# Optimization experiments

Measured on AMD Instinct MI355X. Metric: run time of the kernel, lower is better.

## Reference

```python
import jax, jax.numpy as jnp
import numpy as np

# Conv2d_mvm config (matches init_kwargs): the bit-sliced crossbar MVM is a
# fixed-point emulation of an exact stride-1 conv2d with padding=1, no bias.
C_IN, C_OUT, K, H, W, PAD = 16, 16, 3, 1024, 1024, 1


def setup_inputs() -> dict:
    key = jax.random.key(0)
    kx, kw = jax.random.split(key)
    x = jax.random.normal(kx, (1, C_IN, H, W), dtype=jnp.float32)
    # kaiming_uniform-style init for the conv weight
    fan_in = C_IN * K * K
    bound = 1.0 / np.sqrt(fan_in)
    weight = jax.random.uniform(kw, (C_OUT, C_IN, K, K), dtype=jnp.float32,
                                minval=-bound, maxval=bound)
    return {"x": x, "weight": weight}


def reference(x, weight):
    # Ideal math of the bit-sliced crossbar MVM: per output pixel, the
    # flattened (C_in*K*K) receptive field dotted with each flattened filter.
    out = jax.lax.conv_general_dilated(
        x, weight,
        window_strides=(1, 1),
        padding=((PAD, PAD), (PAD, PAD)),
        dimension_numbers=("NCHW", "OIHW", "NCHW"),
    )
    # Original forward returns (C_out, H_out, W_out) with batch=1 assumed.
    return out[0]
```

## Files before the change

### kernel.cpp

```cpp
#include <hip/hip_runtime.h>


#define H 1024
#define W 1024
#define HW (H * W)
#define TW 128
#define TH 4
#define LROWS 6
#define NQ 34
#define NJOBS (LROWS * NQ)
#define LCOLS 130
#define LPITCH (LCOLS * 32)
#define LDS_BYTES (LROWS * LPITCH)

typedef __bf16 bf16x8 __attribute__((ext_vector_type(8)));
typedef float f32x4 __attribute__((ext_vector_type(4)));
typedef unsigned short ushort8 __attribute__((ext_vector_type(8)));
typedef unsigned int uint4v __attribute__((ext_vector_type(4)));

__device__ __host__ inline unsigned short f2bf(float f) {
  unsigned u = __builtin_bit_cast(unsigned, f);
  return (unsigned short)((u + 0x7fffu + ((u >> 16) & 1u)) >> 16);
}

__global__ __launch_bounds__(256) void conv_prep(const float* __restrict__ w,
                                                 unsigned short* __restrict__ wA) {
  int i = blockIdx.x * 256 + threadIdx.x;
  if (i >= 5 * 64 * 8) return;
  int j = i & 7;
  int l = (i >> 3) & 63;
  int p = i >> 9;
  int k = (l >> 4) * 8 + j;
  int t = 2 * p + (k >> 4);
  int ci = k & 15;
  int co = l & 15;
  float v = (t <= 8) ? w[co * 144 + ci * 9 + t] : 0.f;
  wA[i] = f2bf(v);
}

__device__ __forceinline__ void stage_job(int j, const float* __restrict__ x,
                                          int colbase, int rowbase, char* lds) {
  const int ly  = j / NQ;
  const int qx  = j - ly * NQ;
  const int gy  = rowbase - 1 + ly;
  const float rowm = ((unsigned)gy < (unsigned)H) ? 1.f : 0.f;
  const int gyc  = gy < 0 ? 0 : (gy > H - 1 ? H - 1 : gy);
  const int gx0  = colbase - 4 + 4 * qx;
  const int gx0c = gx0 < 0 ? 0 : (gx0 > W - 4 ? W - 4 : gx0);
  const unsigned voff = (unsigned)((gyc * W + gx0c) * 4);

  f32x4 L[16];
  asm volatile(
      "global_load_dwordx4 %0, %8, %9\n\t"
      "global_load_dwordx4 %1, %8, %10\n\t"
      "global_load_dwordx4 %2, %8, %11\n\t"
      "global_load_dwordx4 %3, %8, %12\n\t"
      "global_load_dwordx4 %4, %8, %13\n\t"
      "global_load_dwordx4 %5, %8, %14\n\t"
      "global_load_dwordx4 %6, %8, %15\n\t"
      "global_load_dwordx4 %7, %8, %16\n\t"
      : "=&v"(L[0]), "=&v"(L[1]), "=&v"(L[2]), "=&v"(L[3]),
        "=&v"(L[4]), "=&v"(L[5]), "=&v"(L[6]), "=&v"(L[7])
      : "v"(voff), "s"(x), "s"(x + HW), "s"(x + 2 * HW), "s"(x + 3 * HW),
        "s"(x + 4 * HW), "s"(x + 5 * HW), "s"(x + 6 * HW), "s"(x + 7 * HW));
  asm volatile(
      "global_load_dwordx4 %0, %8, %9\n\t"
      "global_load_dwordx4 %1, %8, %10\n\t"
      "global_load_dwordx4 %2, %8, %11\n\t"
      "global_load_dwordx4 %3, %8, %12\n\t"
      "global_load_dwordx4 %4, %8, %13\n\t"
      "global_load_dwordx4 %5, %8, %14\n\t"
      "global_load_dwordx4 %6, %8, %15\n\t"
      "global_load_dwordx4 %7, %8, %16\n\t"
      : "=&v"(L[8]), "=&v"(L[9]), "=&v"(L[10]), "=&v"(L[11]),
        "=&v"(L[12]), "=&v"(L[13]), "=&v"(L[14]), "=&v"(L[15])
      : "v"(voff), "s"(x + 8 * HW), "s"(x + 9 * HW), "s"(x + 10 * HW),
        "s"(x + 11 * HW), "s"(x + 12 * HW), "s"(x + 13 * HW),
        "s"(x + 14 * HW), "s"(x + 15 * HW));

  asm volatile("s_waitcnt vmcnt(0)" ::: "memory");
  __builtin_amdgcn_sched_barrier(0);

#pragma unroll
  for (int i = 0; i < 4; ++i) {
    const int gx = gx0 + i;
    const int lx = gx - (colbase - 1);
    if ((unsigned)lx < (unsigned)LCOLS) {
      const float fm = rowm * (((unsigned)gx < (unsigned)W) ? 1.f : 0.f);
      const int lb = (ly * LPITCH + lx * 32) ^ (((lx >> 2) & 3) << 4);
#pragma unroll
      for (int h = 0; h < 2; ++h) {
        uint4v d;
#pragma unroll
        for (int p = 0; p < 4; ++p) {
          const unsigned lo = f2bf(L[h * 8 + 2 * p][i] * fm);
          const unsigned hi = f2bf(L[h * 8 + 2 * p + 1][i] * fm);
          d[p] = lo | (hi << 16);
        }
        *(uint4v*)(lds + (lb ^ (h << 4))) = d;
      }
    }
  }
}

__global__ __launch_bounds__(256, 6) void conv_mfma(
    const float* __restrict__ x, const unsigned short* __restrict__ wA,
    float* __restrict__ out) {
  __shared__ __align__(16) char lds[LDS_BYTES];

  const int tid  = threadIdx.x;
  const int lane = tid & 63;
  const int wave = tid >> 6;
  const int m = lane & 15;
  const int q = lane >> 4;
  const int colbase = blockIdx.x * TW;
  const int rowbase = blockIdx.y * TH;

  if (tid < NJOBS) stage_job(tid, x, colbase, rowbase, lds);

  ushort8 wU[5];
#pragma unroll
  for (int p = 0; p < 5; ++p)
    wU[p] = *(const ushort8*)&wA[(p * 64 + lane) * 8];

  int baseaddr[5];
#pragma unroll
  for (int p = 0; p < 5; ++p) {
    int t = 2 * p + (q >> 1);
    int ky = 0, kx = 0;
    if (t <= 8) { ky = t / 3; kx = t - ky * 3; }
    int col = m + kx;
    int b = ky * LPITCH + col * 32 + (q & 1) * 16;
    b ^= ((col >> 2) & 3) << 4;
    baseaddr[p] = b + wave * LPITCH;
  }

  __syncthreads();

#pragma unroll
  for (int g = 0; g < 8; ++g) {
    f32x4 acc = {0.f, 0.f, 0.f, 0.f};
#pragma unroll
    for (int p = 0; p < 5; ++p) {
      ushort8 bU = *(const ushort8*)(lds + (baseaddr[p] + g * 512));
      acc = __builtin_amdgcn_mfma_f32_16x16x32_bf16(
          __builtin_bit_cast(bf16x8, bU),
          __builtin_bit_cast(bf16x8, wU[p]),
          acc, 0, 0, 0);
    }
    const int y  = rowbase + wave;
    const int x0 = colbase + g * 16 + q * 4;
    *(f32x4*)(out + m * HW + y * W + x0) = acc;
  }
}

extern "C" void kernel_launch(void* const* d_in, const int* in_sizes, int n_in,
                              void* d_out, int out_size, void* d_ws, size_t ws_size,
                              hipStream_t stream) {
  const float* x = (const float*)d_in[0];
  const float* w = (const float*)d_in[1];
  float* out = (float*)d_out;
  unsigned short* wA = (unsigned short*)d_ws;

  conv_prep<<<10, 256, 0, stream>>>(w, wA);

  dim3 grid(W / TW, H / TH);
  conv_mfma<<<grid, 256, 0, stream>>>(x, wA, out);
}
```

Measured before the change: 37.29 us.

## Process two row tiles per block and prefetch the second tile during compute

Each block now handles two vertically adjacent 4-row tiles, so the grid is halved. The global loads for the second tile are issued before the first tile's MFMA compute, which hides their latency behind that compute. Weight loads become inline-asm global loads, and explicit waitcnt and s_barrier calls control the LDS reuse between the two tiles. Launch bounds drop from 6 to 4 waves per SIMD, and the partial vmcnt wait assumes the vector-memory counter completes in order while the output stores are still outstanding.

```diff
diff --git a/kernel.cpp b/kernel.cpp
--- a/kernel.cpp
+++ b/kernel.cpp
@@ -6,6 +6,7 @@
 #define HW (H * W)
 #define TW 128
 #define TH 4
+#define NT 2
 #define LROWS 6
 #define NQ 34
 #define NJOBS (LROWS * NQ)
@@ -38,18 +39,9 @@
   wA[i] = f2bf(v);
 }
 
-__device__ __forceinline__ void stage_job(int j, const float* __restrict__ x,
-                                          int colbase, int rowbase, char* lds) {
-  const int ly  = j / NQ;
-  const int qx  = j - ly * NQ;
-  const int gy  = rowbase - 1 + ly;
-  const float rowm = ((unsigned)gy < (unsigned)H) ? 1.f : 0.f;
-  const int gyc  = gy < 0 ? 0 : (gy > H - 1 ? H - 1 : gy);
-  const int gx0  = colbase - 4 + 4 * qx;
-  const int gx0c = gx0 < 0 ? 0 : (gx0 > W - 4 ? W - 4 : gx0);
-  const unsigned voff = (unsigned)((gyc * W + gx0c) * 4);
-
-  f32x4 L[16];
+__device__ __forceinline__ void issue16(f32x4 (&L)[16],
+                                        const float* __restrict__ x,
+                                        unsigned voff) {
   asm volatile(
       "global_load_dwordx4 %0, %8, %9\n\t"
       "global_load_dwordx4 %1, %8, %10\n\t"
@@ -62,7 +54,8 @@
       : "=&v"(L[0]), "=&v"(L[1]), "=&v"(L[2]), "=&v"(L[3]),
         "=&v"(L[4]), "=&v"(L[5]), "=&v"(L[6]), "=&v"(L[7])
       : "v"(voff), "s"(x), "s"(x + HW), "s"(x + 2 * HW), "s"(x + 3 * HW),
-        "s"(x + 4 * HW), "s"(x + 5 * HW), "s"(x + 6 * HW), "s"(x + 7 * HW));
+        "s"(x + 4 * HW), "s"(x + 5 * HW), "s"(x + 6 * HW), "s"(x + 7 * HW)
+      : "memory");
   asm volatile(
       "global_load_dwordx4 %0, %8, %9\n\t"
       "global_load_dwordx4 %1, %8, %10\n\t"
@@ -76,11 +69,12 @@
         "=&v"(L[12]), "=&v"(L[13]), "=&v"(L[14]), "=&v"(L[15])
       : "v"(voff), "s"(x + 8 * HW), "s"(x + 9 * HW), "s"(x + 10 * HW),
         "s"(x + 11 * HW), "s"(x + 12 * HW), "s"(x + 13 * HW),
-        "s"(x + 14 * HW), "s"(x + 15 * HW));
-
-  asm volatile("s_waitcnt vmcnt(0)" ::: "memory");
-  __builtin_amdgcn_sched_barrier(0);
-
+        "s"(x + 14 * HW), "s"(x + 15 * HW)
+      : "memory");
+}
+
+__device__ __forceinline__ void pack16(const f32x4 (&L)[16], float rowm, int ly,
+                                       int gx0, int colbase, char* lds) {
 #pragma unroll
   for (int i = 0; i < 4; ++i) {
     const int gx = gx0 + i;
@@ -103,7 +97,7 @@
   }
 }
 
-__global__ __launch_bounds__(256, 6) void conv_mfma(
+__global__ __launch_bounds__(256, 4) void conv_mfma(
     const float* __restrict__ x, const unsigned short* __restrict__ wA,
     float* __restrict__ out) {
   __shared__ __align__(16) char lds[LDS_BYTES];
@@ -113,15 +107,43 @@
   const int wave = tid >> 6;
   const int m = lane & 15;
   const int q = lane >> 4;
-  const int colbase = blockIdx.x * TW;
-  const int rowbase = blockIdx.y * TH;
-
-  if (tid < NJOBS) stage_job(tid, x, colbase, rowbase, lds);
+  const int colbase  = blockIdx.x * TW;
+  const int rowbase0 = blockIdx.y * (TH * NT);
+
+  const bool st = tid < NJOBS;
+  int ly = 0, gx0 = 0, gx0c = 0;
+  if (st) {
+    ly = tid / NQ;
+    const int qx = tid - ly * NQ;
+    gx0  = colbase - 4 + 4 * qx;
+    gx0c = gx0 < 0 ? 0 : (gx0 > W - 4 ? W - 4 : gx0);
+  }
+  auto tile_off = [&](int rowbase, float& rm) -> unsigned {
+    const int gy = rowbase - 1 + ly;
+    rm = ((unsigned)gy < (unsigned)H) ? 1.f : 0.f;
+    const int gyc = gy < 0 ? 0 : (gy > H - 1 ? H - 1 : gy);
+    return (unsigned)((gyc * W + gx0c) * 4);
+  };
+
+  f32x4 L[16];
+  float rowm;
+  const unsigned voff0 = tile_off(rowbase0, rowm);
+  if (st) issue16(L, x, voff0);
 
   ushort8 wU[5];
-#pragma unroll
-  for (int p = 0; p < 5; ++p)
-    wU[p] = *(const ushort8*)&wA[(p * 64 + lane) * 8];
+  {
+    const unsigned wvoff = (unsigned)(lane * 16);
+    asm volatile(
+        "global_load_dwordx4 %0, %5, %6\n\t"
+        "global_load_dwordx4 %1, %5, %7\n\t"
+        "global_load_dwordx4 %2, %5, %8\n\t"
+        "global_load_dwordx4 %3, %5, %9\n\t"
+        "global_load_dwordx4 %4, %5, %10\n\t"
+        : "=&v"(wU[0]), "=&v"(wU[1]), "=&v"(wU[2]), "=&v"(wU[3]), "=&v"(wU[4])
+        : "v"(wvoff), "s"(wA), "s"(wA + 512), "s"(wA + 1024), "s"(wA + 1536),
+          "s"(wA + 2048)
+        : "memory");
+  }
 
   int baseaddr[5];
 #pragma unroll
@@ -135,23 +157,42 @@
     baseaddr[p] = b + wave * LPITCH;
   }
 
-  __syncthreads();
-
-#pragma unroll
-  for (int g = 0; g < 8; ++g) {
-    f32x4 acc = {0.f, 0.f, 0.f, 0.f};
-#pragma unroll
-    for (int p = 0; p < 5; ++p) {
-      ushort8 bU = *(const ushort8*)(lds + (baseaddr[p] + g * 512));
-      acc = __builtin_amdgcn_mfma_f32_16x16x32_bf16(
-          __builtin_bit_cast(bf16x8, bU),
-          __builtin_bit_cast(bf16x8, wU[p]),
-          acc, 0, 0, 0);
-    }
-    const int y  = rowbase + wave;
-    const int x0 = colbase + g * 16 + q * 4;
-    *(f32x4*)(out + m * HW + y * W + x0) = acc;
-  }
+  asm volatile("s_waitcnt vmcnt(0)" ::: "memory");
+  __builtin_amdgcn_sched_barrier(0);
+  if (st) pack16(L, rowm, ly, gx0, colbase, lds);
+  asm volatile("s_waitcnt lgkmcnt(0)" ::: "memory");
+  asm volatile("s_barrier" ::: "memory");
+
+#define COMPUTE(RB)                                                         \
+  {                                                                         \
+    const int y = (RB) + wave;                                              \
+    float* const orow = out + m * HW + y * W + colbase + q * 4;             \
+    _Pragma("unroll") for (int g = 0; g < 8; ++g) {                         \
+      f32x4 acc = {0.f, 0.f, 0.f, 0.f};                                     \
+      _Pragma("unroll") for (int p = 0; p < 5; ++p) {                       \
+        const ushort8 bU =                                                  \
+            *(const ushort8*)(lds + (baseaddr[p] + g * 512));               \
+        acc = __builtin_amdgcn_mfma_f32_16x16x32_bf16(                      \
+            __builtin_bit_cast(bf16x8, bU),                \
+            __builtin_bit_cast(bf16x8, wU[p]),             \
+            acc, 0, 0, 0);                                                  \
+      }                                                                     \
+      *(f32x4*)(orow + g * 16) = acc;                                       \
+    }                                                                       \
+  }
+
+  const unsigned voff1 = tile_off(rowbase0 + TH, rowm);
+  if (st) issue16(L, x, voff1);
+  COMPUTE(rowbase0);
+  asm volatile("s_barrier" ::: "memory");
+  asm volatile("s_waitcnt vmcnt(8)" ::: "memory");
+  __builtin_amdgcn_sched_barrier(0);
+  if (st) pack16(L, rowm, ly, gx0, colbase, lds);
+  asm volatile("s_waitcnt lgkmcnt(0)" ::: "memory");
+  asm volatile("s_barrier" ::: "memory");
+  COMPUTE(rowbase0 + TH);
+
+#undef COMPUTE
 }
 
 extern "C" void kernel_launch(void* const* d_in, const int* in_sizes, int n_in,
@@ -164,6 +205,6 @@
 
   conv_prep<<<10, 256, 0, stream>>>(w, wA);
 
-  dim3 grid(W / TW, H / TH);
+  dim3 grid(W / TW, H / (TH * NT));
   conv_mfma<<<grid, 256, 0, stream>>>(x, wA, out);
 }
```

Result: slower. 43.54 us (+16.8%).
